# Optimization experiments

Measured on AMD Instinct MI355X. Metric: run time of the kernel, lower is better.

## Reference

```python
import jax, jax.numpy as jnp
import numpy as np

NUM_QUBITS = 12
ENC_COPIES = 1
ANSATZ_COPIES = 2
BATCH = 1024
NUM_THETAS = NUM_QUBITS * (ANSATZ_COPIES + 1) * 2  # 72

_H = jnp.asarray(np.array([[1.0, 1.0], [1.0, -1.0]], np.complex64) / np.sqrt(2.0))


def _apply_1q(state, U, q):
    # state: [B, 2, 2, ..., 2] (n qubit axes); apply 2x2 unitary U on qubit q
    s = jnp.moveaxis(state, 1 + q, -1)
    s = jnp.einsum('...j,ij->...i', s, U)
    return jnp.moveaxis(s, -1, 1 + q)


def _apply_zpow(state, t, q):
    # cirq Z**t = diag(1, e^{i*pi*t}); t is scalar or per-batch [B]
    n = state.ndim - 1
    phase = jnp.exp(1j * jnp.pi * t).astype(jnp.complex64)
    factor = jnp.stack([jnp.ones_like(phase), phase], axis=-1)
    if factor.ndim == 2:  # batched exponent -> broadcast over other qubit axes
        factor = factor.reshape((factor.shape[0],) + (1,) * (n - 1) + (2,))
    s = jnp.moveaxis(state, 1 + q, -1)
    return jnp.moveaxis(s * factor, -1, 1 + q)


def _ypow_unitary(t):
    # cirq Y**t up to global phase e^{i*pi*t/2} (irrelevant for Z expectations)
    a = 0.5 * jnp.pi * t
    c, s = jnp.cos(a), jnp.sin(a)
    return jnp.stack([jnp.stack([c, -s]), jnp.stack([s, c])]).astype(jnp.complex64)


def _apply_cnot(state, c, t):
    s = jnp.moveaxis(state, (1 + c, 1 + t), (-2, -1))
    s = jnp.stack([s[..., 0, :], s[..., 1, ::-1]], axis=-2)
    return jnp.moveaxis(s, (-2, -1), (1 + c, 1 + t))


def _encoding_block(state, x):
    # FirstOrderPauliZEncoding: per copy, per qubit: H then Z**x_q
    for _ in range(ENC_COPIES):
        for q in range(NUM_QUBITS):
            state = _apply_1q(state, _H, q)
            state = _apply_zpow(state, x[:, q], q)
    return state


def _ansatz_block(state, th, with_cnot):
    # EfficientSU2 layer: Y**th[q,0], Z**th[q,1] per qubit, then CNOT chain
    for q in range(NUM_QUBITS):
        state = _apply_1q(state, _ypow_unitary(th[q, 0]), q)
        state = _apply_zpow(state, th[q, 1], q)
    if with_cnot:
        for q in range(NUM_QUBITS - 1):
            state = _apply_cnot(state, q, q + 1)
    return state


_enc = jax.checkpoint(_encoding_block)
_ans_cnot = jax.checkpoint(lambda st, th: _ansatz_block(st, th, True))
_ans_last = jax.checkpoint(lambda st, th: _ansatz_block(st, th, False))


def _circuit(inputs, thetas):
    b = inputs.shape[0]
    state = jnp.zeros((b, 2 ** NUM_QUBITS), jnp.complex64).at[:, 0].set(1.0)
    state = state.reshape((b,) + (2,) * NUM_QUBITS)
    state = _enc(state, inputs)
    th = thetas.reshape(ANSATZ_COPIES + 1, NUM_QUBITS, 2)
    for l in range(ANSATZ_COPIES + 1):
        state = (_ans_cnot if l < ANSATZ_COPIES else _ans_last)(state, th[l])
    # readouts: <Z_q> for each qubit
    probs = state.real ** 2 + state.imag ** 2
    exps = []
    for q in range(NUM_QUBITS):
        axes = tuple(a for a in range(1, NUM_QUBITS + 1) if a != 1 + q)
        p = probs.sum(axis=axes)  # [B, 2]
        exps.append(p[:, 0] - p[:, 1])
    return jnp.stack(exps, axis=-1)  # [B, NUM_QUBITS]


def setup_inputs() -> dict:
    key = jax.random.key(0)
    k1, k2 = jax.random.split(key)
    inputs = jax.random.uniform(k1, (BATCH, NUM_QUBITS), jnp.float32)
    thetas = jax.random.uniform(k2, (NUM_THETAS,), jnp.float32, minval=-1.0, maxval=1.0)
    return {"inputs": inputs, "thetas": thetas}


def reference(inputs, thetas):
    return _circuit(inputs, thetas)
```

## Files before the change

### kernel.cpp

```cpp
#include <hip/hip_runtime.h>


#define PI_F 3.14159265358979323846f
#define NR 16
#define ROWP_AB 66

__device__ __forceinline__ float2 cmul(float2 a, float2 b) {
    return make_float2(a.x*b.x - a.y*b.y, a.x*b.y + a.y*b.x);
}

template<int RB>
__device__ __forceinline__ void ypow_reg(float2 (&a)[NR], float c, float s) {
    #pragma unroll
    for (int r0 = 0; r0 < NR; ++r0) {
        if ((r0 >> RB) & 1) continue;
        const int r1 = r0 | (1 << RB);
        float2 a0 = a[r0], a1 = a[r1];
        a[r0] = make_float2(c*a0.x - s*a1.x, c*a0.y - s*a1.y);
        a[r1] = make_float2(s*a0.x + c*a1.x, s*a0.y + c*a1.y);
    }
}

__device__ __forceinline__ void exchange_BA(float2 (&a)[NR], float2* buf,
                                            int w, int lane,
                                            float c0, float s0, float c1, float s1,
                                            bool first) {
    if (!first) __syncthreads();
    {
        const int x9 = lane >> 5;
        const int v0 = (w >> 1) & 1;
        const int v1 = v0 ^ (w & 1);
        const int wbase = x9 * 2176 + v1 * 1088 + v0 * 544 + (lane & 31) * 17;
        #pragma unroll
        for (int r = 0; r < NR; ++r)
            buf[wbase + r] = a[r];
    }
    __syncthreads();
    const float y0a = (w & 2) ? s0 : c0;
    const float y0b = (w & 2) ? c0 : -s0;
    const float y1a = (w & 1) ? s1 : c1;
    const float y1b = (w & 1) ? c1 : -s1;
    const float K00 = y0a*y1a, K01 = y0a*y1b, K10 = y0b*y1a, K11 = y0b*y1b;
    #pragma unroll
    for (int rp = 0; rp < NR; ++rp) {
        const int ylow = (rp << 6) | lane;
        const int t = (ylow ^ (ylow >> 1)) & 511;
        const int y9 = (rp >> 3) & 1;
        const int gbase = ((t >> 4) & 31) * 17 + (t & 15);
        float2 i00 = buf[ y9      * 2176           + gbase];
        float2 i10 = buf[ y9      * 2176 +     544 + gbase];
        float2 i01 = buf[(y9 ^ 1) * 2176 + 1088    + gbase];
        float2 i11 = buf[(y9 ^ 1) * 2176 + 1632    + gbase];
        a[rp] = make_float2(K00*i00.x + K01*i01.x + K10*i10.x + K11*i11.x,
                            K00*i00.y + K01*i01.y + K10*i10.y + K11*i11.y);
    }
}

__device__ __forceinline__ void exchange_AB(float2 (&a)[NR], float2* wbuf,
                                            int lane,
                                            float c6, float s6, float c7, float s7) {
    __syncthreads();
    const int wslot = (lane & 15) * 4 + (lane >> 4);
    #pragma unroll
    for (int r = 0; r < NR; ++r)
        wbuf[r * ROWP_AB + wslot] = a[r];
    const int j = lane & 3;
    const float e0 = (j & 2) ? s6 : c6;
    const float e1 = (j & 2) ? c6 : -s6;
    const float f0 = (j & 1) ? s7 : c7;
    const float f1 = (j & 1) ? c7 : -s7;
    const float C0 = e0*f0, C1 = e0*f1, C2 = e1*f0, C3 = e1*f1;
    const int rbase = (lane >> 2) * ROWP_AB;
    #pragma unroll
    for (int rp = 0; rp < NR; ++rp) {
        float2 p0 = wbuf[rbase + rp * 4 + 0];
        float2 p1 = wbuf[rbase + rp * 4 + 1];
        float2 p2 = wbuf[rbase + rp * 4 + 2];
        float2 p3 = wbuf[rbase + rp * 4 + 3];
        a[rp] = make_float2(C0*p0.x + C1*p1.x + C2*p2.x + C3*p3.x,
                            C0*p0.y + C1*p1.y + C2*p2.y + C3*p3.y);
    }
}

__device__ __forceinline__ void fused_z_B(float2 (&a)[NR], int w, int lane,
                                          const float* __restrict__ th) {
    float alpha = 0.0f;
    if (w & 2) alpha += th[1];
    if (w & 1) alpha += th[3];
    #pragma unroll
    for (int k = 0; k < 6; ++k)
        alpha += ((lane >> k) & 1) ? th[2*(7-k)+1] : 0.0f;
    float2 cA; __sincosf(PI_F * alpha, &cA.y, &cA.x);
    float2 z8, z9, z10, z11;
    __sincosf(PI_F * th[17], &z8.y,  &z8.x);
    __sincosf(PI_F * th[19], &z9.y,  &z9.x);
    __sincosf(PI_F * th[21], &z10.y, &z10.x);
    __sincosf(PI_F * th[23], &z11.y, &z11.x);
    float2 hi[4], lo[4];
    hi[0] = cA;                    hi[1] = cmul(cA, z9);
    hi[2] = cmul(cA, z8);          hi[3] = cmul(hi[2], z9);
    lo[0] = make_float2(1.f, 0.f); lo[1] = z11;
    lo[2] = z10;                   lo[3] = cmul(z10, z11);
    #pragma unroll
    for (int r = 0; r < NR; ++r)
        a[r] = cmul(cmul(a[r], hi[r >> 2]), lo[r & 3]);
}

__device__ __forceinline__ void encode_init(float2 (&a)[NR], int w, int lane,
                                            const float* __restrict__ x,
                                            const float* __restrict__ th0) {
    float2 F = make_float2(0.015625f, 0.0f);
    #pragma unroll
    for (int q = 0; q < 8; ++q) {
        float2 ex; __sincosf(PI_F * x[q], &ex.y, &ex.x);
        float sy, cy; __sincosf(0.5f * PI_F * th0[2*q], &sy, &cy);
        float2 cz; __sincosf(PI_F * th0[2*q+1], &cz.y, &cz.x);
        float2 u0 = make_float2(cy - sy*ex.x, -sy*ex.y);
        float2 u1 = cmul(cz, make_float2(sy + cy*ex.x, cy*ex.y));
        int bit;
        if (q == 0)      bit = (w >> 1) & 1;
        else if (q == 1) bit = w & 1;
        else             bit = (lane >> (7 - q)) & 1;
        F = cmul(F, bit ? u1 : u0);
    }
    float2 v0[4], v1[4];
    #pragma unroll
    for (int q = 8; q < 12; ++q) {
        float2 ex; __sincosf(PI_F * x[q], &ex.y, &ex.x);
        float sy, cy; __sincosf(0.5f * PI_F * th0[2*q], &sy, &cy);
        float2 cz; __sincosf(PI_F * th0[2*q+1], &cz.y, &cz.x);
        v0[q-8] = make_float2(cy - sy*ex.x, -sy*ex.y);
        v1[q-8] = cmul(cz, make_float2(sy + cy*ex.x, cy*ex.y));
    }
    float2 hi[4], lo[4];
    hi[0] = cmul(v0[0], v0[1]); hi[1] = cmul(v0[0], v1[1]);
    hi[2] = cmul(v1[0], v0[1]); hi[3] = cmul(v1[0], v1[1]);
    lo[0] = cmul(v0[2], v0[3]); lo[1] = cmul(v0[2], v1[3]);
    lo[2] = cmul(v1[2], v0[3]); lo[3] = cmul(v1[2], v1[3]);
    #pragma unroll
    for (int t = 0; t < 4; ++t) hi[t] = cmul(F, hi[t]);
    #pragma unroll
    for (int r = 0; r < NR; ++r)
        a[r] = cmul(hi[r >> 2], lo[r & 3]);
}

__global__ __launch_bounds__(256) void vqc_kernel(
    const float* __restrict__ inputs,
    const float* __restrict__ thetas,
    float* __restrict__ out)
{
    __shared__ __align__(16) float2 buf[4352];
    __shared__ float redBuf[4][12];

    const int b = blockIdx.x;
    const int tid = threadIdx.x;
    const int w = tid >> 6;
    const int lane = tid & 63;
    const float* x = inputs + b * 12;
    const float* th1 = thetas + 24;
    const float* th2 = thetas + 48;

    float2 a[NR];
    encode_init(a, w, lane, x, thetas);

    { float s0,c0,s1,c1;
      __sincosf(0.5f*PI_F*th1[0], &s0, &c0);
      __sincosf(0.5f*PI_F*th1[2], &s1, &c1);
      exchange_BA(a, buf, w, lane, c0, s0, c1, s1, true); }

    { float s,c; __sincosf(0.5f*PI_F*th1[4],  &s,&c); ypow_reg<3>(a,c,s); }
    { float s,c; __sincosf(0.5f*PI_F*th1[6],  &s,&c); ypow_reg<2>(a,c,s); }
    { float s,c; __sincosf(0.5f*PI_F*th1[8],  &s,&c); ypow_reg<1>(a,c,s); }
    { float s,c; __sincosf(0.5f*PI_F*th1[10], &s,&c); ypow_reg<0>(a,c,s); }
    { float s6,c6,s7,c7;
      __sincosf(0.5f*PI_F*th1[12], &s6,&c6);
      __sincosf(0.5f*PI_F*th1[14], &s7,&c7);
      exchange_AB(a, buf + w * (NR * ROWP_AB), lane, c6, s6, c7, s7); }
    { float s,c; __sincosf(0.5f*PI_F*th1[16], &s,&c); ypow_reg<3>(a,c,s); }
    { float s,c; __sincosf(0.5f*PI_F*th1[18], &s,&c); ypow_reg<2>(a,c,s); }
    { float s,c; __sincosf(0.5f*PI_F*th1[20], &s,&c); ypow_reg<1>(a,c,s); }
    { float s,c; __sincosf(0.5f*PI_F*th1[22], &s,&c); ypow_reg<0>(a,c,s); }
    fused_z_B(a, w, lane, th1);

    { float s0,c0,s1,c1;
      __sincosf(0.5f*PI_F*th2[0], &s0, &c0);
      __sincosf(0.5f*PI_F*th2[2], &s1, &c1);
      exchange_BA(a, buf, w, lane, c0, s0, c1, s1, false); }

    { float s,c; __sincosf(0.5f*PI_F*th2[4],  &s,&c); ypow_reg<3>(a,c,s); }
    { float s,c; __sincosf(0.5f*PI_F*th2[6],  &s,&c); ypow_reg<2>(a,c,s); }
    { float s,c; __sincosf(0.5f*PI_F*th2[8],  &s,&c); ypow_reg<1>(a,c,s); }
    { float s,c; __sincosf(0.5f*PI_F*th2[10], &s,&c); ypow_reg<0>(a,c,s); }
    { float s6,c6,s7,c7;
      __sincosf(0.5f*PI_F*th2[12], &s6,&c6);
      __sincosf(0.5f*PI_F*th2[14], &s7,&c7);
      exchange_AB(a, buf + w * (NR * ROWP_AB), lane, c6, s6, c7, s7); }
    { float s,c; __sincosf(0.5f*PI_F*th2[16], &s,&c); ypow_reg<3>(a,c,s); }
    { float s,c; __sincosf(0.5f*PI_F*th2[18], &s,&c); ypow_reg<2>(a,c,s); }
    { float s,c; __sincosf(0.5f*PI_F*th2[20], &s,&c); ypow_reg<1>(a,c,s); }
    { float s,c; __sincosf(0.5f*PI_F*th2[22], &s,&c); ypow_reg<0>(a,c,s); }

    float totalP = 0.0f;
    float D[4] = {0, 0, 0, 0};
    #pragma unroll
    for (int r = 0; r < NR; ++r) {
        const float p = a[r].x * a[r].x + a[r].y * a[r].y;
        totalP += p;
        #pragma unroll
        for (int j = 0; j < 4; ++j)
            D[j] += ((r >> j) & 1) ? -p : p;
    }
    #pragma unroll
    for (int q = 0; q < 12; ++q) {
        float v;
        if (q == 0)      v = (w & 2) ? -totalP : totalP;
        else if (q == 1) v = (w & 1) ? -totalP : totalP;
        else if (q <= 7) v = ((lane >> (7 - q)) & 1) ? -totalP : totalP;
        else             v = D[11 - q];
        #pragma unroll
        for (int off = 32; off >= 1; off >>= 1)
            v += __shfl_xor(v, off, 64);
        if (lane == 0) redBuf[w][q] = v;
    }
    __syncthreads();
    if (tid < 12)
        out[b * 12 + tid] = redBuf[0][tid] + redBuf[1][tid]
                          + redBuf[2][tid] + redBuf[3][tid];
}

extern "C" void kernel_launch(void* const* d_in, const int* in_sizes, int n_in,
                              void* d_out, int out_size, void* d_ws, size_t ws_size,
                              hipStream_t stream) {
    const float* inputs = (const float*)d_in[0];
    const float* thetas = (const float*)d_in[1];
    float* out = (float*)d_out;
    vqc_kernel<<<dim3(1024), dim3(256), 0, stream>>>(inputs, thetas, out);
}
```

Baseline: 78.39 us.

## Pack shared-memory exchanges as fp16, use swizzled layouts and split buffers

Both register-exchange stages now store amplitudes as packed half2 in LDS with XOR-swizzled layouts, so each output reads its four taps with a single 128-bit load. The AB exchange gets its own buffer, which removes one block-wide barrier. The Z-readout reduction is restructured into butterfly shuffles that share partial sums instead of running twelve full 64-lane reductions. Rounding the state to fp16 at every exchange lowers accuracy and may exceed the comparison tolerance.

```diff
diff --git a/kernel.cpp b/kernel.cpp
--- a/kernel.cpp
+++ b/kernel.cpp
@@ -3,8 +3,19 @@
 
 #define PI_F 3.14159265358979323846f
 #define NR 16
-#define ROWP_AB 66
-
+
+typedef _Float16 half2v __attribute__((ext_vector_type(2)));
+
+__device__ __forceinline__ unsigned packh(float2 a) {
+    half2v h; h.x = (_Float16)a.x; h.y = (_Float16)a.y;
+    return __builtin_bit_cast(unsigned, h);
+}
+__device__ __forceinline__ float lo16(unsigned u) {
+    return (float)__builtin_bit_cast(half2v, u).x;
+}
+__device__ __forceinline__ float hi16(unsigned u) {
+    return (float)__builtin_bit_cast(half2v, u).y;
+}
 __device__ __forceinline__ float2 cmul(float2 a, float2 b) {
     return make_float2(a.x*b.x - a.y*b.y, a.x*b.y + a.y*b.x);
 }
@@ -21,19 +32,20 @@
     }
 }
 
-__device__ __forceinline__ void exchange_BA(float2 (&a)[NR], float2* buf,
+__device__ __forceinline__ void exchange_BA(float2 (&a)[NR], unsigned* buf,
                                             int w, int lane,
                                             float c0, float s0, float c1, float s1,
                                             bool first) {
     if (!first) __syncthreads();
     {
-        const int x9 = lane >> 5;
         const int v0 = (w >> 1) & 1;
         const int v1 = v0 ^ (w & 1);
-        const int wbase = x9 * 2176 + v1 * 1088 + v0 * 544 + (lane & 31) * 17;
+        const int u  = (lane >> 5) ^ v1;
+        const int tap = (v1 << 1) | v0;
+        const int gx = ((u << 9) | ((lane & 31) << 4)) ^ (lane & 31);
         #pragma unroll
         for (int r = 0; r < NR; ++r)
-            buf[wbase + r] = a[r];
+            buf[((gx ^ r) << 2) | tap] = packh(a[r]);
     }
     __syncthreads();
     const float y0a = (w & 2) ? s0 : c0;
@@ -45,40 +57,37 @@
     for (int rp = 0; rp < NR; ++rp) {
         const int ylow = (rp << 6) | lane;
         const int t = (ylow ^ (ylow >> 1)) & 511;
-        const int y9 = (rp >> 3) & 1;
-        const int gbase = ((t >> 4) & 31) * 17 + (t & 15);
-        float2 i00 = buf[ y9      * 2176           + gbase];
-        float2 i10 = buf[ y9      * 2176 +     544 + gbase];
-        float2 i01 = buf[(y9 ^ 1) * 2176 + 1088    + gbase];
-        float2 i11 = buf[(y9 ^ 1) * 2176 + 1632    + gbase];
-        a[rp] = make_float2(K00*i00.x + K01*i01.x + K10*i10.x + K11*i11.x,
-                            K00*i00.y + K01*i01.y + K10*i10.y + K11*i11.y);
-    }
-}
-
-__device__ __forceinline__ void exchange_AB(float2 (&a)[NR], float2* wbuf,
+        const int g = ((rp >> 3) << 9) | t;
+        const int gp = g ^ (t >> 4);
+        const uint4 d = *(const uint4*)(buf + (gp << 2));
+        a[rp].x = K00*lo16(d.x) + K01*lo16(d.z) + K10*lo16(d.y) + K11*lo16(d.w);
+        a[rp].y = K00*hi16(d.x) + K01*hi16(d.z) + K10*hi16(d.y) + K11*hi16(d.w);
+    }
+}
+
+__device__ __forceinline__ void exchange_AB(float2 (&a)[NR], unsigned* wbuf,
                                             int lane,
                                             float c6, float s6, float c7, float s7) {
-    __syncthreads();
-    const int wslot = (lane & 15) * 4 + (lane >> 4);
-    #pragma unroll
-    for (int r = 0; r < NR; ++r)
-        wbuf[r * ROWP_AB + wslot] = a[r];
+    {
+        const int tap = lane >> 4;
+        const int m = lane & 15;
+        #pragma unroll
+        for (int r = 0; r < NR; ++r)
+            wbuf[(((r << 4) | (m ^ r)) << 2) | tap] = packh(a[r]);
+    }
     const int j = lane & 3;
     const float e0 = (j & 2) ? s6 : c6;
     const float e1 = (j & 2) ? c6 : -s6;
     const float f0 = (j & 1) ? s7 : c7;
     const float f1 = (j & 1) ? c7 : -s7;
     const float C0 = e0*f0, C1 = e0*f1, C2 = e1*f0, C3 = e1*f1;
-    const int rbase = (lane >> 2) * ROWP_AB;
+    const int row = lane >> 2;
     #pragma unroll
     for (int rp = 0; rp < NR; ++rp) {
-        float2 p0 = wbuf[rbase + rp * 4 + 0];
-        float2 p1 = wbuf[rbase + rp * 4 + 1];
-        float2 p2 = wbuf[rbase + rp * 4 + 2];
-        float2 p3 = wbuf[rbase + rp * 4 + 3];
-        a[rp] = make_float2(C0*p0.x + C1*p1.x + C2*p2.x + C3*p3.x,
-                            C0*p0.y + C1*p1.y + C2*p2.y + C3*p3.y);
+        const int gp = (row << 4) | (rp ^ row);
+        const uint4 d = *(const uint4*)(wbuf + (gp << 2));
+        a[rp].x = C0*lo16(d.x) + C1*lo16(d.y) + C2*lo16(d.z) + C3*lo16(d.w);
+        a[rp].y = C0*hi16(d.x) + C1*hi16(d.y) + C2*hi16(d.z) + C3*hi16(d.w);
     }
 }
 
@@ -149,7 +158,8 @@
     const float* __restrict__ thetas,
     float* __restrict__ out)
 {
-    __shared__ __align__(16) float2 buf[4352];
+    __shared__ __align__(16) unsigned bufBA[4096];
+    __shared__ __align__(16) unsigned bufAB[4096];
     __shared__ float redBuf[4][12];
 
     const int b = blockIdx.x;
@@ -166,7 +176,7 @@
     { float s0,c0,s1,c1;
       __sincosf(0.5f*PI_F*th1[0], &s0, &c0);
       __sincosf(0.5f*PI_F*th1[2], &s1, &c1);
-      exchange_BA(a, buf, w, lane, c0, s0, c1, s1, true); }
+      exchange_BA(a, bufBA, w, lane, c0, s0, c1, s1, true); }
 
     { float s,c; __sincosf(0.5f*PI_F*th1[4],  &s,&c); ypow_reg<3>(a,c,s); }
     { float s,c; __sincosf(0.5f*PI_F*th1[6],  &s,&c); ypow_reg<2>(a,c,s); }
@@ -175,7 +185,7 @@
     { float s6,c6,s7,c7;
       __sincosf(0.5f*PI_F*th1[12], &s6,&c6);
       __sincosf(0.5f*PI_F*th1[14], &s7,&c7);
-      exchange_AB(a, buf + w * (NR * ROWP_AB), lane, c6, s6, c7, s7); }
+      exchange_AB(a, bufAB + w * 1024, lane, c6, s6, c7, s7); }
     { float s,c; __sincosf(0.5f*PI_F*th1[16], &s,&c); ypow_reg<3>(a,c,s); }
     { float s,c; __sincosf(0.5f*PI_F*th1[18], &s,&c); ypow_reg<2>(a,c,s); }
     { float s,c; __sincosf(0.5f*PI_F*th1[20], &s,&c); ypow_reg<1>(a,c,s); }
@@ -185,7 +195,7 @@
     { float s0,c0,s1,c1;
       __sincosf(0.5f*PI_F*th2[0], &s0, &c0);
       __sincosf(0.5f*PI_F*th2[2], &s1, &c1);
-      exchange_BA(a, buf, w, lane, c0, s0, c1, s1, false); }
+      exchange_BA(a, bufBA, w, lane, c0, s0, c1, s1, false); }
 
     { float s,c; __sincosf(0.5f*PI_F*th2[4],  &s,&c); ypow_reg<3>(a,c,s); }
     { float s,c; __sincosf(0.5f*PI_F*th2[6],  &s,&c); ypow_reg<2>(a,c,s); }
@@ -194,33 +204,50 @@
     { float s6,c6,s7,c7;
       __sincosf(0.5f*PI_F*th2[12], &s6,&c6);
       __sincosf(0.5f*PI_F*th2[14], &s7,&c7);
-      exchange_AB(a, buf + w * (NR * ROWP_AB), lane, c6, s6, c7, s7); }
+      exchange_AB(a, bufAB + w * 1024, lane, c6, s6, c7, s7); }
     { float s,c; __sincosf(0.5f*PI_F*th2[16], &s,&c); ypow_reg<3>(a,c,s); }
     { float s,c; __sincosf(0.5f*PI_F*th2[18], &s,&c); ypow_reg<2>(a,c,s); }
     { float s,c; __sincosf(0.5f*PI_F*th2[20], &s,&c); ypow_reg<1>(a,c,s); }
     { float s,c; __sincosf(0.5f*PI_F*th2[22], &s,&c); ypow_reg<0>(a,c,s); }
 
-    float totalP = 0.0f;
-    float D[4] = {0, 0, 0, 0};
+    float P = 0.0f, D0 = 0, D1 = 0, D2 = 0, D3 = 0;
     #pragma unroll
     for (int r = 0; r < NR; ++r) {
         const float p = a[r].x * a[r].x + a[r].y * a[r].y;
-        totalP += p;
+        P += p;
+        D0 += (r & 1) ? -p : p;
+        D1 += (r & 2) ? -p : p;
+        D2 += (r & 4) ? -p : p;
+        D3 += (r & 8) ? -p : p;
+    }
+    float f[6];
+    float m = P;
+    #pragma unroll
+    for (int k = 0; k < 6; ++k) {
+        float p = __shfl_xor(m, 32 >> k, 64);
+        f[k] = m - p;
+        m = m + p;
+    }
+    #pragma unroll
+    for (int k = 0; k < 6; ++k) {
         #pragma unroll
-        for (int j = 0; j < 4; ++j)
-            D[j] += ((r >> j) & 1) ? -p : p;
-    }
-    #pragma unroll
-    for (int q = 0; q < 12; ++q) {
-        float v;
-        if (q == 0)      v = (w & 2) ? -totalP : totalP;
-        else if (q == 1) v = (w & 1) ? -totalP : totalP;
-        else if (q <= 7) v = ((lane >> (7 - q)) & 1) ? -totalP : totalP;
-        else             v = D[11 - q];
-        #pragma unroll
-        for (int off = 32; off >= 1; off >>= 1)
-            v += __shfl_xor(v, off, 64);
-        if (lane == 0) redBuf[w][q] = v;
+        for (int s = 16 >> k; s >= 1; s >>= 1)
+            f[k] += __shfl_xor(f[k], s, 64);
+    }
+    #pragma unroll
+    for (int s = 32; s >= 1; s >>= 1) {
+        D0 += __shfl_xor(D0, s, 64);
+        D1 += __shfl_xor(D1, s, 64);
+        D2 += __shfl_xor(D2, s, 64);
+        D3 += __shfl_xor(D3, s, 64);
+    }
+    if (lane == 0) {
+        float* rb = redBuf[w];
+        rb[0] = (w & 2) ? -m : m;
+        rb[1] = (w & 1) ? -m : m;
+        rb[2] = f[0]; rb[3] = f[1]; rb[4] = f[2];
+        rb[5] = f[3]; rb[6] = f[4]; rb[7] = f[5];
+        rb[8] = D3; rb[9] = D2; rb[10] = D1; rb[11] = D0;
     }
     __syncthreads();
     if (tid < 12)
```

Result: no change. 78.03 us (-0.4%).
